# Performance work log

Measured on AMD Instinct MI355X. Metric: run time of the kernel, lower is better.

Reference implementation:

```python
import jax, jax.numpy as jnp
import numpy as np

B, H, W, C = 16, 64, 64, 192
NUM_HEADS, KEY_DIM, KS = 8, 32, 3


def setup_inputs() -> dict:
    key = jax.random.key(0)
    ks = jax.random.split(key, 9)
    Ck = C + 2  # key/value input dim: patches concat 2 dist channels
    def w(k, shape, fan_in):
        return jax.random.normal(k, shape, jnp.float32) / np.float32(np.sqrt(fan_in))
    return {
        "x": jax.random.normal(ks[0], (B, H, W, C), jnp.float32),
        "Wq": w(ks[1], (C, NUM_HEADS, KEY_DIM), C),
        "bq": jnp.zeros((NUM_HEADS, KEY_DIM), jnp.float32),
        "Wk": w(ks[2], (Ck, NUM_HEADS, KEY_DIM), Ck),
        "bk": jnp.zeros((NUM_HEADS, KEY_DIM), jnp.float32),
        "Wv": w(ks[3], (Ck, NUM_HEADS, KEY_DIM), Ck),
        "bv": jnp.zeros((NUM_HEADS, KEY_DIM), jnp.float32),
        "Wo": w(ks[4], (NUM_HEADS, KEY_DIM, C), NUM_HEADS * KEY_DIM),
        "bo": jnp.zeros((C,), jnp.float32),
    }


def _local_window_kv(x, ks):
    # tf.image.extract_patches SAME (zero pad) -> [B,H,W,ks*ks,C]
    pad = ks // 2
    xp = jnp.pad(x, ((0, 0), (pad, pad), (pad, pad), (0, 0)))
    b, h, w, c = x.shape
    patches = jnp.stack(
        [xp[:, i:i + h, j:j + w, :] for i in range(ks) for j in range(ks)], axis=3
    )  # [B,H,W,ks*ks,C], row-major over window like extract_patches
    # relative distances: tf.meshgrid default 'xy', concat (dists[0], dists[1])
    r = jnp.arange(ks, dtype=x.dtype) - ks // 2
    dx, dy = jnp.meshgrid(r, r)  # 'xy' indexing, matches tf.meshgrid default
    dists = jnp.stack([dx, dy], axis=-1).reshape(ks * ks, 2)  # [9,2]
    dists = jnp.broadcast_to(dists, (b, h, w, ks * ks, 2))
    return jnp.concatenate([patches, dists], axis=-1)  # [B,H,W,9,C+2]


def reference(x, Wq, bq, Wk, bk, Wv, bv, Wo, bo):
    kv_in = _local_window_kv(x, KS)  # [B,H,W,9,C+2]
    # keras MultiHeadAttention projections
    q = jnp.einsum('bxyc,chd->bxyhd', x, Wq) + bq           # [B,H,W,h,d] (q_len=1)
    k = jnp.einsum('bxykc,chd->bxykhd', kv_in, Wk) + bk     # [B,H,W,9,h,d]
    v = jnp.einsum('bxykc,chd->bxykhd', kv_in, Wv) + bv
    scale = np.float32(1.0 / np.sqrt(KEY_DIM))
    scores = jnp.einsum('bxyhd,bxykhd->bxyhk', q, k) * scale  # [B,H,W,h,9]
    attn = jax.nn.softmax(scores, axis=-1)
    o = jnp.einsum('bxyhk,bxykhd->bxyhd', attn, v)
    return jnp.einsum('bxyhd,hdc->bxyc', o, Wo) + bo          # [B,H,W,C]
```

## Files before the change

### kernel.cpp

```cpp
#include <hip/hip_runtime.h>
#include <hip/hip_bf16.h>


typedef __bf16 bf16x8_t __attribute__((ext_vector_type(8)));
typedef float f32x4_t __attribute__((ext_vector_type(4)));

#define SCALE 0.17677669529663687f
#define QSTRIDE 864
#define ZROW 65536

static __device__ __forceinline__ unsigned short bfbits(float f) {
    return __builtin_bit_cast(unsigned short, __float2bfloat16(f));
}
static __device__ __forceinline__ float bf2f(unsigned short u) {
    return __bfloat162float(__builtin_bit_cast(__hip_bfloat16, u));
}
static __device__ __forceinline__ float lo16f(unsigned int u) {
    return __builtin_bit_cast(float, u << 16);
}
static __device__ __forceinline__ float hi16f(unsigned int u) {
    return __builtin_bit_cast(float, u & 0xffff0000u);
}

static __device__ __forceinline__ void gload_lds16(const void* g, void* l) {
    __builtin_amdgcn_global_load_lds((const __attribute__((address_space(1))) void*)g,
                                     (__attribute__((address_space(3))) void*)l, 16, 0, 0);
}

__global__ void k_convert_x(const float* __restrict__ x, ushort4* __restrict__ xb, int n4) {
    int i = blockIdx.x * blockDim.x + threadIdx.x;
    const int stride = gridDim.x * blockDim.x;
    const float4* x4 = reinterpret_cast<const float4*>(x);
    for (; i < n4; i += stride) {
        float4 v = x4[i];
        ushort4 o;
        o.x = bfbits(v.x); o.y = bfbits(v.y); o.z = bfbits(v.z); o.w = bfbits(v.w);
        xb[i] = o;
    }
}

__global__ void k_pack(const float* __restrict__ Wq, const float* __restrict__ Wk,
                       const float* __restrict__ Wv, const float* __restrict__ Wo,
                       const float* __restrict__ bq, const float* __restrict__ bk,
                       const float* __restrict__ bv,
                       __hip_bfloat16* __restrict__ WqkvT, __hip_bfloat16* __restrict__ WoT,
                       float* __restrict__ qkvBias, float* __restrict__ wvTab,
                       __hip_bfloat16* __restrict__ QKV) {
    const int idx = blockIdx.x * blockDim.x + threadIdx.x;
    const int T0 = 896 * 192;
    const int T1 = T0 + 192 * 256;
    const int T2 = T1 + 896;
    const int T3 = T2 + 768;
    const int T4 = T3 + QSTRIDE;
    if (idx < T0) {
        const int m = idx / 192, k = idx % 192;
        float v = 0.f;
        if (m < 256) {
            v = Wq[k * 256 + m] * SCALE;
        } else if (m < 768) {
            const int j = m - 256, g = j >> 3, r = j & 7;
            const int d = 4 * g + (r & 3);
            v = (r < 4) ? Wk[k * 256 + d] : Wv[k * 256 + d];
        } else if (m < 864) {
            const int j = m - 768, h = j / 12, n = j % 12;
            if (n < 9) {
                const float dj = (float)(n % 3 - 1), di = (float)(n / 3 - 1);
                float acc = 0.f;
                for (int d = 0; d < 32; ++d) {
                    const int c = h * 32 + d;
                    const float bkv = dj * Wk[192 * 256 + c] + di * Wk[193 * 256 + c] + bk[c];
                    acc += Wq[k * 256 + c] * bkv;
                }
                v = acc * SCALE;
            }
        }
        WqkvT[m * 192 + k] = __float2bfloat16(v);
    } else if (idx < T1) {
        const int j = idx - T0;
        const int c = j >> 8, hd = j & 255;
        WoT[j] = __float2bfloat16(Wo[hd * 192 + c]);
    } else if (idx < T2) {
        const int col = idx - T1;
        float v = 0.f;
        if (col < 256) v = bq[col] * SCALE;
        else if (col >= 768 && col < 864) {
            const int j = col - 768, h = j / 12, n = j % 12;
            if (n < 9) {
                const float dj = (float)(n % 3 - 1), di = (float)(n / 3 - 1);
                float acc = 0.f;
                for (int d = 0; d < 32; ++d) {
                    const int c = h * 32 + d;
                    const float bkv = dj * Wk[192 * 256 + c] + di * Wk[193 * 256 + c] + bk[c];
                    acc += bq[c] * bkv;
                }
                v = acc * SCALE;
            }
        }
        qkvBias[col] = v;
    } else if (idx < T3) {
        const int j = idx - T2;
        const int t = j >> 8, m = j & 255;
        float v;
        if (t == 0)      v = Wv[192 * 256 + m];
        else if (t == 1) v = Wv[193 * 256 + m];
        else             v = bv[m];
        wvTab[j] = v;
    } else if (idx < T4) {
        const int j = idx - T3;
        QKV[(size_t)ZROW * QSTRIDE + j] = __float2bfloat16(0.f);
    }
}

template<int BM, int BN, int WRN, int WCN, int KDIM, int NOUT, int NBX, bool OUTF32, bool BIAS>
__global__ __launch_bounds__(64 * WRN * WCN) void k_gemm_lds(const __hip_bfloat16* __restrict__ A,
                          const __hip_bfloat16* __restrict__ BT,
                          void* __restrict__ Cout,
                          const float* __restrict__ bias, int ldc) {
    constexpr int NW = WRN * WCN;
    constexpr int WTR = BM / WRN;
    constexpr int WTC = BN / WCN;
    constexpr int FR = WTR / 16;
    constexpr int FC = WTC / 16;
    constexpr int NK = KDIM / 64;
    __shared__ __hip_bfloat16 sA[BM * 64];
    __shared__ __hip_bfloat16 sB[BN * 64];
    const int bid = blockIdx.x;
    const int s = (bid & 7) * ((int)gridDim.x >> 3) + (bid >> 3);
    const int by = s / NBX, bx = s - by * NBX;
    const int tid = threadIdx.x;
    const int wave = tid >> 6, lane = tid & 63;
    const int wr = wave / WCN, wc = wave % WCN;
    const long rowBase = (long)by * BM;
    const long colBase = (long)bx * BN;
    const int lr = lane & 15, lk = lane >> 4;
    const int rx = lr & 7;
    const int srow = lane >> 3;
    const int scolsw = ((lane & 7) ^ srow) * 8;

    f32x4_t acc[FR][FC] = {};
    for (int t = 0; t < NK; ++t) {
        const int k0 = t * 64;
        #pragma unroll
        for (int r = 0; r < BM / (8 * NW); ++r) {
            const int row0 = r * (8 * NW) + wave * 8;
            gload_lds16(A + (rowBase + row0 + srow) * KDIM + k0 + scolsw, sA + row0 * 64);
        }
        #pragma unroll
        for (int r = 0; r < BN / (8 * NW) + ((BN % (8 * NW)) ? 1 : 0); ++r) {
            const int row0 = r * (8 * NW) + wave * 8;
            if (row0 < BN)
                gload_lds16(BT + (colBase + row0 + srow) * KDIM + k0 + scolsw, sB + row0 * 64);
        }
        __syncthreads();
        #pragma unroll
        for (int kk = 0; kk < 2; ++kk) {
            const int pc = ((lk + kk * 4) ^ rx) * 8;
            bf16x8_t a[FR], b[FC];
            #pragma unroll
            for (int fr = 0; fr < FR; ++fr)
                a[fr] = *reinterpret_cast<const bf16x8_t*>(sA + (wr * WTR + fr * 16 + lr) * 64 + pc);
            #pragma unroll
            for (int fc = 0; fc < FC; ++fc)
                b[fc] = *reinterpret_cast<const bf16x8_t*>(sB + (wc * WTC + fc * 16 + lr) * 64 + pc);
            #pragma unroll
            for (int fr = 0; fr < FR; ++fr) {
                #pragma unroll
                for (int fc = 0; fc < FC; ++fc)
                    acc[fr][fc] = __builtin_amdgcn_mfma_f32_16x16x32_bf16(a[fr], b[fc], acc[fr][fc], 0, 0, 0);
            }
        }
        __syncthreads();
    }
    const int rowSub = (lane >> 4) * 4;
    const int colSub = lane & 15;
    #pragma unroll
    for (int fr = 0; fr < FR; ++fr) {
        #pragma unroll
        for (int fc = 0; fc < FC; ++fc) {
            const long col = colBase + wc * WTC + fc * 16 + colSub;
            if (col >= NOUT) continue;
            float bvv = BIAS ? bias[col] : 0.f;
            #pragma unroll
            for (int r = 0; r < 4; ++r) {
                const long row = rowBase + wr * WTR + fr * 16 + rowSub + r;
                float v = acc[fr][fc][r] + bvv;
                if constexpr (OUTF32) ((float*)Cout)[row * ldc + col] = v;
                else ((__hip_bfloat16*)Cout)[row * ldc + col] = __float2bfloat16(v);
            }
        }
    }
}

__global__ __launch_bounds__(256) void k_attn(const __hip_bfloat16* __restrict__ QKV,
                       const float* __restrict__ wvTab,
                       __hip_bfloat16* __restrict__ O) {
    const int wave = threadIdx.x >> 6;
    const int lane = threadIdx.x & 63;
    const int bid = blockIdx.x;
    const int sblk = (bid & 7) * 512 + (bid >> 3);
    const int qd = sblk * 4 + wave;
    const int b = qd >> 10;
    const int qy = (qd >> 5) & 31, qx = qd & 31;
    const int y = qy << 1, x = qx << 1;
    const int p00 = (b << 12) | (y << 6) | x;
    const int h = lane >> 3, dg = lane & 7;
    const int idx = h * 32 + dg * 4;
    const char* baseQ = reinterpret_cast<const char*>(QKV);
    const int laneOff = 512 + 128 * h + 16 * dg;

    uint4 kv[16];
    #pragma unroll
    for (int m = 0; m < 16; ++m) {
        const int rr = m >> 2, cc = m & 3;
        const int ny = y + rr - 1, nx = x + cc - 1;
        const bool inb = ((unsigned)ny < 64u) & ((unsigned)nx < 64u);
        const long row = inb ? (long)((b << 12) | (ny << 6) | nx) : (long)ZROW;
        kv[m] = *reinterpret_cast<const uint4*>(baseQ + row * (QSTRIDE * 2) + laneOff);
    }

    ushort4 quA[4], qaA[4], qbvA[4];
    unsigned short qcA[4];
    #pragma unroll
    for (int pxi = 0; pxi < 4; ++pxi) {
        const int dy = pxi >> 1, dx = pxi & 1;
        const __hip_bfloat16* rowQ = QKV + (size_t)(p00 + dy * 64 + dx) * QSTRIDE;
        quA[pxi]  = *reinterpret_cast<const ushort4*>(rowQ + idx);
        qaA[pxi]  = *reinterpret_cast<const ushort4*>(rowQ + 768 + 12 * h);
        qbvA[pxi] = *reinterpret_cast<const ushort4*>(rowQ + 772 + 12 * h);
        qcA[pxi]  = *reinterpret_cast<const unsigned short*>(rowQ + 776 + 12 * h);
    }

    const float4 w0 = *reinterpret_cast<const float4*>(wvTab + idx);
    const float4 w1 = *reinterpret_cast<const float4*>(wvTab + 256 + idx);
    const float4 w2 = *reinterpret_cast<const float4*>(wvTab + 512 + idx);

    #pragma unroll
    for (int pxi = 0; pxi < 4; ++pxi) {
        const int dy = pxi >> 1, dx = pxi & 1;
        const int p = p00 + dy * 64 + dx;
        const ushort4 qu = quA[pxi];
        const ushort4 qa = qaA[pxi];
        const ushort4 qbv = qbvA[pxi];
        const unsigned short qc = qcA[pxi];
        const float q0 = bf2f(qu.x), q1 = bf2f(qu.y), q2 = bf2f(qu.z), q3 = bf2f(qu.w);
        const float qb[9] = { bf2f(qa.x), bf2f(qa.y), bf2f(qa.z), bf2f(qa.w),
                              bf2f(qbv.x), bf2f(qbv.y), bf2f(qbv.z), bf2f(qbv.w), bf2f(qc) };

        float sc[9];
        #pragma unroll
        for (int n = 0; n < 9; ++n) {
            const int m = (dy + n / 3) * 4 + dx + n % 3;
            const uint4 k = kv[m];
            float s = fmaf(q0, lo16f(k.x), fmaf(q1, hi16f(k.x),
                      fmaf(q2, lo16f(k.y), q3 * hi16f(k.y))));
            s += __shfl_xor(s, 1);
            s += __shfl_xor(s, 2);
            s += __shfl_xor(s, 4);
            sc[n] = s + qb[n];
        }
        float mx = sc[0];
        #pragma unroll
        for (int n = 1; n < 9; ++n) mx = fmaxf(mx, sc[n]);
        float sum = 0.f;
        #pragma unroll
        for (int n = 0; n < 9; ++n) { sc[n] = __expf(sc[n] - mx); sum += sc[n]; }
        const float inv = 1.0f / sum;
        const float Ej = (sc[2] + sc[5] + sc[8]) - (sc[0] + sc[3] + sc[6]);
        const float Ei = (sc[6] + sc[7] + sc[8]) - (sc[0] + sc[1] + sc[2]);

        float o0 = 0.f, o1 = 0.f, o2 = 0.f, o3 = 0.f;
        #pragma unroll
        for (int n = 0; n < 9; ++n) {
            const int m = (dy + n / 3) * 4 + dx + n % 3;
            const uint4 k = kv[m];
            o0 = fmaf(sc[n], lo16f(k.z), o0);
            o1 = fmaf(sc[n], hi16f(k.z), o1);
            o2 = fmaf(sc[n], lo16f(k.w), o2);
            o3 = fmaf(sc[n], hi16f(k.w), o3);
        }
        ushort4 ov;
        ov.x = bfbits(fmaf(Ej, w0.x, fmaf(Ei, w1.x, o0)) * inv + w2.x);
        ov.y = bfbits(fmaf(Ej, w0.y, fmaf(Ei, w1.y, o1)) * inv + w2.y);
        ov.z = bfbits(fmaf(Ej, w0.z, fmaf(Ei, w1.z, o2)) * inv + w2.z);
        ov.w = bfbits(fmaf(Ej, w0.w, fmaf(Ei, w1.w, o3)) * inv + w2.w);
        *reinterpret_cast<ushort4*>(O + (size_t)p * 256 + idx) = ov;
    }
}

extern "C" void kernel_launch(void* const* d_in, const int* in_sizes, int n_in,
                              void* d_out, int out_size, void* d_ws, size_t ws_size,
                              hipStream_t stream) {
    (void)in_sizes; (void)n_in; (void)out_size; (void)ws_size;
    const float* x  = (const float*)d_in[0];
    const float* Wq = (const float*)d_in[1];
    const float* bq = (const float*)d_in[2];
    const float* Wk = (const float*)d_in[3];
    const float* bk = (const float*)d_in[4];
    const float* Wv = (const float*)d_in[5];
    const float* bv = (const float*)d_in[6];
    const float* Wo = (const float*)d_in[7];
    const float* bo = (const float*)d_in[8];

    char* ws = (char*)d_ws;
    __hip_bfloat16* xb    = (__hip_bfloat16*)(ws + 0);
    __hip_bfloat16* O     = (__hip_bfloat16*)(ws + 0);
    __hip_bfloat16* QKV   = (__hip_bfloat16*)(ws + 33554432);
    __hip_bfloat16* WqkvT = (__hip_bfloat16*)(ws + 146802368);
    __hip_bfloat16* WoT   = (__hip_bfloat16*)(ws + 147146432);
    float* qkvBias        = (float*)(ws + 147244736);
    float* wvTab          = (float*)(ws + 147248320);

    k_convert_x<<<4096, 256, 0, stream>>>(x, (ushort4*)xb, 12582912 / 4);
    k_pack<<<874, 256, 0, stream>>>(Wq, Wk, Wv, Wo, bq, bk, bv, WqkvT, WoT, qkvBias, wvTab, QKV);
    k_gemm_lds<128, 128, 2, 4, 192, 864, 7, false, true>
        <<<3584, 512, 0, stream>>>(xb, WqkvT, (void*)QKV, qkvBias, QSTRIDE);
    k_attn<<<4096, 256, 0, stream>>>(QKV, wvTab, O);
    k_gemm_lds<128, 64, 2, 4, 256, 192, 3, true, true>
        <<<1536, 512, 0, stream>>>(O, WoT, d_out, bo, 192);
}
```

Baseline: 110.1 us.

## Share 6x6 KV halo across waves via LDS for 4x4 pixel tiles

The attention kernel now assigns each block a 4x4 pixel tile, with each wave handling a 2x2 quadrant. The block loads the 6x6 halo of K/V rows once into shared memory using direct global-to-LDS loads, and each wave reads its 3x3 neighbourhoods from there. Before, every wave fetched its own 4x4 halo from global memory, so halo rows were loaded redundantly across waves. This cuts global K/V traffic but adds LDS use (36KB per block), a barrier, and LDS reads that may limit occupancy.

```diff
diff --git a/kernel.cpp b/kernel.cpp
--- a/kernel.cpp
+++ b/kernel.cpp
@@ -194,36 +194,36 @@
 __global__ __launch_bounds__(256) void k_attn(const __hip_bfloat16* __restrict__ QKV,
                        const float* __restrict__ wvTab,
                        __hip_bfloat16* __restrict__ O) {
+    __shared__ __hip_bfloat16 sKV[36 * 512];
     const int wave = threadIdx.x >> 6;
     const int lane = threadIdx.x & 63;
     const int bid = blockIdx.x;
     const int sblk = (bid & 7) * 512 + (bid >> 3);
-    const int qd = sblk * 4 + wave;
-    const int b = qd >> 10;
-    const int qy = (qd >> 5) & 31, qx = qd & 31;
-    const int y = qy << 1, x = qx << 1;
-    const int p00 = (b << 12) | (y << 6) | x;
+    const int b  = sblk >> 8;
+    const int ty = (sblk >> 4) & 15, tx = sblk & 15;
+    const int y0 = ty << 2, x0 = tx << 2;
+    const int qr = wave >> 1, qc = wave & 1;
     const int h = lane >> 3, dg = lane & 7;
     const int idx = h * 32 + dg * 4;
     const char* baseQ = reinterpret_cast<const char*>(QKV);
-    const int laneOff = 512 + 128 * h + 16 * dg;
-
-    uint4 kv[16];
+
     #pragma unroll
-    for (int m = 0; m < 16; ++m) {
-        const int rr = m >> 2, cc = m & 3;
-        const int ny = y + rr - 1, nx = x + cc - 1;
+    for (int j = 0; j < 9; ++j) {
+        const int pi = wave * 9 + j;
+        const int wr = pi / 6, wc = pi % 6;
+        const int ny = y0 + wr - 1, nx = x0 + wc - 1;
         const bool inb = ((unsigned)ny < 64u) & ((unsigned)nx < 64u);
         const long row = inb ? (long)((b << 12) | (ny << 6) | nx) : (long)ZROW;
-        kv[m] = *reinterpret_cast<const uint4*>(baseQ + row * (QSTRIDE * 2) + laneOff);
+        gload_lds16(baseQ + row * (QSTRIDE * 2) + 512 + lane * 16, sKV + pi * 512);
     }
 
     ushort4 quA[4], qaA[4], qbvA[4];
     unsigned short qcA[4];
     #pragma unroll
     for (int pxi = 0; pxi < 4; ++pxi) {
-        const int dy = pxi >> 1, dx = pxi & 1;
-        const __hip_bfloat16* rowQ = QKV + (size_t)(p00 + dy * 64 + dx) * QSTRIDE;
+        const int py = 2 * qr + (pxi >> 1), px = 2 * qc + (pxi & 1);
+        const int p = (b << 12) | ((y0 + py) << 6) | (x0 + px);
+        const __hip_bfloat16* rowQ = QKV + (size_t)p * QSTRIDE;
         quA[pxi]  = *reinterpret_cast<const ushort4*>(rowQ + idx);
         qaA[pxi]  = *reinterpret_cast<const ushort4*>(rowQ + 768 + 12 * h);
         qbvA[pxi] = *reinterpret_cast<const ushort4*>(rowQ + 772 + 12 * h);
@@ -234,23 +234,32 @@
     const float4 w1 = *reinterpret_cast<const float4*>(wvTab + 256 + idx);
     const float4 w2 = *reinterpret_cast<const float4*>(wvTab + 512 + idx);
 
+    __syncthreads();
+
     #pragma unroll
     for (int pxi = 0; pxi < 4; ++pxi) {
         const int dy = pxi >> 1, dx = pxi & 1;
-        const int p = p00 + dy * 64 + dx;
+        const int py = 2 * qr + dy, px = 2 * qc + dx;
+        const int p = (b << 12) | ((y0 + py) << 6) | (x0 + px);
         const ushort4 qu = quA[pxi];
         const ushort4 qa = qaA[pxi];
         const ushort4 qbv = qbvA[pxi];
-        const unsigned short qc = qcA[pxi];
+        const unsigned short qc2 = qcA[pxi];
         const float q0 = bf2f(qu.x), q1 = bf2f(qu.y), q2 = bf2f(qu.z), q3 = bf2f(qu.w);
         const float qb[9] = { bf2f(qa.x), bf2f(qa.y), bf2f(qa.z), bf2f(qa.w),
-                              bf2f(qbv.x), bf2f(qbv.y), bf2f(qbv.z), bf2f(qbv.w), bf2f(qc) };
+                              bf2f(qbv.x), bf2f(qbv.y), bf2f(qbv.z), bf2f(qbv.w), bf2f(qc2) };
+
+        uint4 kvn[9];
+        #pragma unroll
+        for (int n = 0; n < 9; ++n) {
+            const int pi = (py + n / 3) * 6 + (px + n % 3);
+            kvn[n] = *reinterpret_cast<const uint4*>(sKV + pi * 512 + lane * 8);
+        }
 
         float sc[9];
         #pragma unroll
         for (int n = 0; n < 9; ++n) {
-            const int m = (dy + n / 3) * 4 + dx + n % 3;
-            const uint4 k = kv[m];
+            const uint4 k = kvn[n];
             float s = fmaf(q0, lo16f(k.x), fmaf(q1, hi16f(k.x),
                       fmaf(q2, lo16f(k.y), q3 * hi16f(k.y))));
             s += __shfl_xor(s, 1);
@@ -271,8 +280,7 @@
         float o0 = 0.f, o1 = 0.f, o2 = 0.f, o3 = 0.f;
         #pragma unroll
         for (int n = 0; n < 9; ++n) {
-            const int m = (dy + n / 3) * 4 + dx + n % 3;
-            const uint4 k = kv[m];
+            const uint4 k = kvn[n];
             o0 = fmaf(sc[n], lo16f(k.z), o0);
             o1 = fmaf(sc[n], hi16f(k.z), o1);
             o2 = fmaf(sc[n], lo16f(k.w), o2);
```

New measurement: 117.5 us. 6.7% more time.
